# Performance work log

Hardware: AMD Instinct MI355X
Metric: run time of the kernel (lower is better)

## Reference

```python
import jax, jax.numpy as jnp
import numpy as np

B, L, D, N, K = 4, 4096, 1024, 64, 3
EPS = 1e-6

def setup_inputs() -> dict:
    key = jax.random.key(0)
    ks = jax.random.split(key, 24)
    f32 = jnp.float32
    inp = {
        'T': jax.random.normal(ks[0], (B, L, D), f32),
        'norm_scale': jnp.ones((D,), f32),
        'in_w': jax.random.normal(ks[1], (2 * D, D), f32) * (1.0 / np.sqrt(D)),
        'in_b': jnp.zeros((2 * D,), f32),
        'dw_w': jax.random.normal(ks[2], (D, 1, K), f32) * (1.0 / np.sqrt(K)),
        'dw_b': jnp.zeros((D,), f32),
        'pw_w': jax.random.normal(ks[3], (D, D), f32) * (1.0 / np.sqrt(D)),
        'pw_b': jnp.zeros((D,), f32),
        'f_win': jax.random.normal(ks[4], (N, D), f32) * (1.0 / np.sqrt(D)),
        'f_wout': jax.random.normal(ks[5], (D, N), f32) * (1.0 / np.sqrt(N)),
        'f_logA': jax.random.normal(ks[6], (N,), f32) * 0.02,
        'f_B': jax.random.normal(ks[7], (N,), f32) * 0.02,
        'f_C': jax.random.normal(ks[8], (N,), f32) * 0.02,
        'f_logdt': jnp.array(0.0, f32),
        'b_win': jax.random.normal(ks[9], (N, D), f32) * (1.0 / np.sqrt(D)),
        'b_wout': jax.random.normal(ks[10], (D, N), f32) * (1.0 / np.sqrt(N)),
        'b_logA': jax.random.normal(ks[11], (N,), f32) * 0.02,
        'b_B': jax.random.normal(ks[12], (N,), f32) * 0.02,
        'b_C': jax.random.normal(ks[13], (N,), f32) * 0.02,
        'b_logdt': jnp.array(0.0, f32),
        'out_w': jax.random.normal(ks[14], (D, D), f32) * (1.0 / np.sqrt(D)),
        'out_b': jnp.zeros((D,), f32),
    }
    return inp

def _ssm(x, win, wout, logA, Bp, Cp, logdt):
    # ZOH discretization of diagonal SSM
    dt = jnp.exp(logdt)
    A = -jnp.exp(logA)
    Abar = jnp.exp(A * dt)
    denom = jnp.where(jnp.abs(A) < EPS, jnp.ones_like(A), A)
    frac = jnp.where(jnp.abs(A) < EPS, dt, (Abar - 1.0) / denom)
    Bbar = frac * Bp
    u = jnp.einsum('bld,nd->bln', x, win)  # (B,L,N)
    h0 = jnp.zeros((x.shape[0], win.shape[0]), x.dtype)
    def step(h, ut):
        h = h * Abar + ut * Bbar
        return h, h * Cp
    _, ys = jax.lax.scan(step, h0, jnp.swapaxes(u, 0, 1))  # (L,B,N)
    y = jnp.swapaxes(ys, 0, 1)
    return jnp.einsum('bln,dn->bld', y, wout)

def reference(T, norm_scale, in_w, in_b, dw_w, dw_b, pw_w, pw_b,
              f_win, f_wout, f_logA, f_B, f_C, f_logdt,
              b_win, b_wout, b_logA, b_B, b_C, b_logdt,
              out_w, out_b):
    # RMSNorm
    rms = jnp.sqrt(jnp.mean(T * T, axis=-1, keepdims=True) + EPS)
    Tn = T / rms * norm_scale
    # in_linear -> chunk
    xz = Tn @ in_w.T + in_b
    x, z = jnp.split(xz, 2, axis=-1)
    gate = jax.nn.sigmoid(z)
    # depthwise-separable conv1d (NCH layout)
    xc = jnp.swapaxes(x, 1, 2)  # (B,D,L)
    xc = jax.lax.conv_general_dilated(
        xc, dw_w, window_strides=(1,), padding=[(K // 2, K // 2)],
        dimension_numbers=('NCH', 'OIH', 'NCH'), feature_group_count=D)
    xc = xc + dw_b[None, :, None]
    xc = jnp.einsum('bdl,ed->bel', xc, pw_w) + pw_b[None, :, None]
    x_conv = jnp.swapaxes(xc, 1, 2)  # (B,L,D)
    # bidirectional SSM
    y_f = _ssm(x_conv, f_win, f_wout, f_logA, f_B, f_C, f_logdt)
    y_b = _ssm(jnp.flip(x_conv, axis=1), b_win, b_wout, b_logA, b_B, b_C, b_logdt)
    y_b = jnp.flip(y_b, axis=1)
    y = (y_f + y_b) * gate
    y = y @ out_w.T + out_b
    return T + y
```

## Files before the change

### kernel.cpp

```cpp
#include <hip/hip_runtime.h>
#include <cstdint>


#define L_SEQ 4096
#define D_DIM 1024
#define B_SZ 4
#define M_TOK (B_SZ * L_SEQ)
#define CHUNKS 64
#define CLEN (L_SEQ / CHUNKS)

typedef short bf16x8 __attribute__((ext_vector_type(8)));
typedef float floatx4 __attribute__((ext_vector_type(4)));

__device__ inline unsigned short f2bf(float f) {
  union { float f; unsigned int u; } v; v.f = f;
  unsigned int r = v.u + 0x7FFFu + ((v.u >> 16) & 1u);
  return (unsigned short)(r >> 16);
}
__device__ inline float bf2f(unsigned short h) {
  union { unsigned int u; float f; } v; v.u = ((unsigned int)h) << 16;
  return v.f;
}

__device__ inline void load_lds16(const unsigned short* g, unsigned short* l) {
  __builtin_amdgcn_global_load_lds(
      (const __attribute__((address_space(1))) unsigned int*)g,
      (__attribute__((address_space(3))) unsigned int*)l, 16, 0, 0);
}

__global__ __launch_bounds__(256) void rmsnorm_kernel(
    const float* __restrict__ T, const float* __restrict__ scale,
    unsigned short* __restrict__ Tn) {
  int tok = blockIdx.x;
  int t = threadIdx.x;
  const float4* row = (const float4*)(T + (size_t)tok * D_DIM);
  float4 v = row[t];
  float ss = v.x*v.x + v.y*v.y + v.z*v.z + v.w*v.w;
  #pragma unroll
  for (int off = 32; off > 0; off >>= 1) ss += __shfl_down(ss, off);
  __shared__ float part[4];
  if ((t & 63) == 0) part[t >> 6] = ss;
  __syncthreads();
  float total = part[0] + part[1] + part[2] + part[3];
  float rinv = rsqrtf(total * (1.0f / D_DIM) + 1e-6f);
  const float4* sc4 = (const float4*)scale;
  float4 s = sc4[t];
  ushort4 o;
  o.x = f2bf(v.x * rinv * s.x); o.y = f2bf(v.y * rinv * s.y);
  o.z = f2bf(v.z * rinv * s.z); o.w = f2bf(v.w * rinv * s.w);
  ((ushort4*)(Tn + (size_t)tok * D_DIM))[t] = o;
}

__global__ __launch_bounds__(256) void f2bf_vec_kernel(
    const float* __restrict__ in, unsigned short* __restrict__ out, int n4) {
  int i = blockIdx.x * 256 + threadIdx.x;
  if (i < n4) {
    float4 v = ((const float4*)in)[i];
    ushort4 o; o.x = f2bf(v.x); o.y = f2bf(v.y); o.z = f2bf(v.z); o.w = f2bf(v.w);
    ((ushort4*)out)[i] = o;
  }
}

__global__ void prepack_kernel(
    const float* __restrict__ f_win, const float* __restrict__ b_win,
    const float* __restrict__ f_wout, const float* __restrict__ b_wout,
    unsigned short* __restrict__ Wu, unsigned short* __restrict__ Wy) {
  int i = blockIdx.x * blockDim.x + threadIdx.x;
  if (i < 128 * D_DIM) {
    int n = i >> 10, k = i & (D_DIM - 1);
    Wu[i] = f2bf((n < 64) ? f_win[n * D_DIM + k] : b_win[(n - 64) * D_DIM + k]);
    int d = i >> 7, kk = i & 127;
    Wy[i] = f2bf((kk < 64) ? f_wout[d * 64 + kk] : b_wout[d * 64 + (kk - 64)]);
  }
}

template<int MODE, typename OUT_T>
__global__ __launch_bounds__(256) void gemm_mfma_kernel(
    const unsigned short* __restrict__ A, const unsigned short* __restrict__ Bw,
    const float* __restrict__ bias, OUT_T* __restrict__ out,
    int M, int N, int Kt,
    const float* __restrict__ aux0, float* __restrict__ aux1) {
  __shared__ unsigned short As[128 * 32];
  __shared__ unsigned short Bs[128 * 32];
  int tid = threadIdx.x;
  int wave = tid >> 6, lane = tid & 63;
  int quad = lane >> 4, lrow = lane & 15;
  int bm = blockIdx.x * 128, bn = blockIdx.y * 128;
  int wm = (wave & 1) * 64, wn = (wave >> 1) * 64;

  int r0 = tid >> 2;
  int c8 = (tid & 3) * 8;
  const unsigned short* Ag0 = A  + (size_t)(bm + r0) * Kt + c8;
  const unsigned short* Ag1 = A  + (size_t)(bm + 64 + r0) * Kt + c8;
  const unsigned short* Bg0 = Bw + (size_t)(bn + r0) * Kt + c8;
  const unsigned short* Bg1 = Bw + (size_t)(bn + 64 + r0) * Kt + c8;
  unsigned short* Al0 = As + (size_t)(wave * 64) * 8;
  unsigned short* Al1 = As + (size_t)(256 + wave * 64) * 8;
  unsigned short* Bl0 = Bs + (size_t)(wave * 64) * 8;
  unsigned short* Bl1 = Bs + (size_t)(256 + wave * 64) * 8;

  floatx4 acc[4][4] = {};
  for (int k0 = 0; k0 < Kt; k0 += 32) {
    load_lds16(Ag0 + k0, Al0);
    load_lds16(Ag1 + k0, Al1);
    load_lds16(Bg0 + k0, Bl0);
    load_lds16(Bg1 + k0, Bl1);
    __syncthreads();
    bf16x8 af[4], bfr[4];
    #pragma unroll
    for (int mi = 0; mi < 4; ++mi)
      af[mi] = *(const bf16x8*)(As + (wm + mi * 16 + lrow) * 32 + quad * 8);
    #pragma unroll
    for (int ni = 0; ni < 4; ++ni)
      bfr[ni] = *(const bf16x8*)(Bs + (wn + ni * 16 + lrow) * 32 + quad * 8);
    #pragma unroll
    for (int mi = 0; mi < 4; ++mi)
      #pragma unroll
      for (int ni = 0; ni < 4; ++ni)
        acc[mi][ni] = __builtin_amdgcn_mfma_f32_16x16x32_bf16(
            af[mi], bfr[ni], acc[mi][ni], 0, 0, 0);
    __syncthreads();
  }

  #pragma unroll
  for (int mi = 0; mi < 4; ++mi) {
    #pragma unroll
    for (int ni = 0; ni < 4; ++ni) {
      #pragma unroll
      for (int r = 0; r < 4; ++r) {
        int m = bm + wm + mi * 16 + quad * 4 + r;
        int n = bn + wn + ni * 16 + lrow;
        float v = acc[mi][ni][r];
        if (MODE == 0) {
          if (bias) v += bias[n];
          if (sizeof(OUT_T) == 2) out[(size_t)m * N + n] = (OUT_T)f2bf(v);
          else                    out[(size_t)m * N + n] = (OUT_T)v;
        } else if (MODE == 1) {
          if (bias) v += bias[n];
          if (n < D_DIM) ((unsigned short*)out)[(size_t)m * D_DIM + n] = f2bf(v);
          else aux1[(size_t)m * D_DIM + (n - D_DIM)] = 1.0f / (1.0f + expf(-v));
        } else if (MODE == 2) {
          v *= aux0[(size_t)m * N + n];
          ((unsigned short*)out)[(size_t)m * N + n] = f2bf(v);
        } else {
          if (bias) v += bias[n];
          v += aux0[(size_t)m * N + n];
          ((float*)out)[(size_t)m * N + n] = v;
        }
      }
    }
  }
}

__global__ __launch_bounds__(256) void dwconv_kernel(
    const unsigned short* __restrict__ x, const float* __restrict__ w,
    const float* __restrict__ b, unsigned short* __restrict__ out) {
  size_t i8 = (size_t)blockIdx.x * 256 + threadIdx.x;
  int d8 = (int)(i8 & (D_DIM / 8 - 1));
  size_t tok = i8 >> 7;
  int l = (int)(tok & (L_SEQ - 1));
  int d0 = d8 * 8;
  size_t base = tok * D_DIM + d0;
  bf16x8 cur = *(const bf16x8*)(x + base);
  float acc[8];
  #pragma unroll
  for (int j = 0; j < 8; ++j) {
    int d = d0 + j;
    acc[j] = b[d] + w[d * 3 + 1] * bf2f((unsigned short)cur[j]);
  }
  if (l > 0) {
    bf16x8 prv = *(const bf16x8*)(x + base - D_DIM);
    #pragma unroll
    for (int j = 0; j < 8; ++j) acc[j] += w[(d0 + j) * 3 + 0] * bf2f((unsigned short)prv[j]);
  }
  if (l < L_SEQ - 1) {
    bf16x8 nxt = *(const bf16x8*)(x + base + D_DIM);
    #pragma unroll
    for (int j = 0; j < 8; ++j) acc[j] += w[(d0 + j) * 3 + 2] * bf2f((unsigned short)nxt[j]);
  }
  bf16x8 o;
  #pragma unroll
  for (int j = 0; j < 8; ++j) o[j] = (short)f2bf(acc[j]);
  *(bf16x8*)(out + base) = o;
}

__device__ inline void ssm_params(
    int col,
    const float* f_logA, const float* f_B, const float* f_C, const float* f_logdt,
    const float* b_logA, const float* b_B, const float* b_C, const float* b_logdt,
    float& Abar, float& Bbar, float& Cc, float& Aa, float& dt) {
  int dir = col >> 6, n = col & 63;
  const float* logA  = dir ? b_logA  : f_logA;
  const float* Bp    = dir ? b_B     : f_B;
  const float* Cp    = dir ? b_C     : f_C;
  const float* logdt = dir ? b_logdt : f_logdt;
  dt = expf(logdt[0]);
  Aa = -expf(logA[n]);
  Abar = expf(Aa * dt);
  float frac = (fabsf(Aa) < 1e-6f) ? dt : (Abar - 1.0f) / Aa;
  Bbar = frac * Bp[n];
  Cc = Cp[n];
}

__global__ __launch_bounds__(128) void scan_s1_kernel(
    const float* __restrict__ u, float* __restrict__ states,
    const float* __restrict__ f_logA, const float* __restrict__ f_B,
    const float* __restrict__ f_C, const float* __restrict__ f_logdt,
    const float* __restrict__ b_logA, const float* __restrict__ b_B,
    const float* __restrict__ b_C, const float* __restrict__ b_logdt) {
  int col = threadIdx.x;
  int chunk = blockIdx.x, b = blockIdx.y;
  float Abar, Bbar, Cc, Aa, dt;
  ssm_params(col, f_logA, f_B, f_C, f_logdt, b_logA, b_B, b_C, b_logdt,
             Abar, Bbar, Cc, Aa, dt);
  size_t base = ((size_t)b * L_SEQ + (size_t)chunk * CLEN) * 128 + col;
  float h = 0.0f;
  if (col < 64) {
    for (int i0 = 0; i0 < CLEN; i0 += 8) {
      float uv[8];
      #pragma unroll
      for (int j = 0; j < 8; ++j) uv[j] = u[base + (size_t)(i0 + j) * 128];
      #pragma unroll
      for (int j = 0; j < 8; ++j) h = h * Abar + uv[j] * Bbar;
    }
  } else {
    for (int i0 = CLEN - 1; i0 >= 0; i0 -= 8) {
      float uv[8];
      #pragma unroll
      for (int j = 0; j < 8; ++j) uv[j] = u[base + (size_t)(i0 - j) * 128];
      #pragma unroll
      for (int j = 0; j < 8; ++j) h = h * Abar + uv[j] * Bbar;
    }
  }
  states[((size_t)b * CHUNKS + chunk) * 128 + col] = h;
}

__global__ __launch_bounds__(512) void scan_s2_kernel(
    const float* __restrict__ states, float* __restrict__ carries,
    const float* __restrict__ f_logA, const float* __restrict__ f_B,
    const float* __restrict__ f_C, const float* __restrict__ f_logdt,
    const float* __restrict__ b_logA, const float* __restrict__ b_B,
    const float* __restrict__ b_C, const float* __restrict__ b_logdt) {
  int tid = threadIdx.x;
  int b = tid >> 7, col = tid & 127;
  float Abar, Bbar, Cc, Aa, dt;
  ssm_params(col, f_logA, f_B, f_C, f_logdt, b_logA, b_B, b_C, b_logdt,
             Abar, Bbar, Cc, Aa, dt);
  float Ac = expf(Aa * dt * (float)CLEN);
  size_t sb = (size_t)b * CHUNKS * 128 + col;
  float cur = 0.0f;
  if (col < 64) {
    for (int c = 0; c < CHUNKS; ++c) {
      carries[sb + (size_t)c * 128] = cur;
      cur = cur * Ac + states[sb + (size_t)c * 128];
    }
  } else {
    for (int c = CHUNKS - 1; c >= 0; --c) {
      carries[sb + (size_t)c * 128] = cur;
      cur = cur * Ac + states[sb + (size_t)c * 128];
    }
  }
}

__global__ __launch_bounds__(128) void scan_s3_kernel(
    const float* __restrict__ u, const float* __restrict__ carries,
    unsigned short* __restrict__ y,
    const float* __restrict__ f_logA, const float* __restrict__ f_B,
    const float* __restrict__ f_C, const float* __restrict__ f_logdt,
    const float* __restrict__ b_logA, const float* __restrict__ b_B,
    const float* __restrict__ b_C, const float* __restrict__ b_logdt) {
  int col = threadIdx.x;
  int chunk = blockIdx.x, b = blockIdx.y;
  float Abar, Bbar, Cc, Aa, dt;
  ssm_params(col, f_logA, f_B, f_C, f_logdt, b_logA, b_B, b_C, b_logdt,
             Abar, Bbar, Cc, Aa, dt);
  size_t base = ((size_t)b * L_SEQ + (size_t)chunk * CLEN) * 128 + col;
  float h = carries[((size_t)b * CHUNKS + chunk) * 128 + col];
  if (col < 64) {
    for (int i0 = 0; i0 < CLEN; i0 += 8) {
      float uv[8];
      #pragma unroll
      for (int j = 0; j < 8; ++j) uv[j] = u[base + (size_t)(i0 + j) * 128];
      #pragma unroll
      for (int j = 0; j < 8; ++j) {
        h = h * Abar + uv[j] * Bbar;
        y[base + (size_t)(i0 + j) * 128] = f2bf(h * Cc);
      }
    }
  } else {
    for (int i0 = CLEN - 1; i0 >= 0; i0 -= 8) {
      float uv[8];
      #pragma unroll
      for (int j = 0; j < 8; ++j) uv[j] = u[base + (size_t)(i0 - j) * 128];
      #pragma unroll
      for (int j = 0; j < 8; ++j) {
        h = h * Abar + uv[j] * Bbar;
        y[base + (size_t)(i0 - j) * 128] = f2bf(h * Cc);
      }
    }
  }
}

extern "C" void kernel_launch(void* const* d_in, const int* in_sizes, int n_in,
                              void* d_out, int out_size, void* d_ws, size_t ws_size,
                              hipStream_t stream) {
  const float* T         = (const float*)d_in[0];
  const float* norm_scale= (const float*)d_in[1];
  const float* in_w      = (const float*)d_in[2];
  const float* in_b      = (const float*)d_in[3];
  const float* dw_w      = (const float*)d_in[4];
  const float* dw_b      = (const float*)d_in[5];
  const float* pw_w      = (const float*)d_in[6];
  const float* pw_b      = (const float*)d_in[7];
  const float* f_win     = (const float*)d_in[8];
  const float* f_wout    = (const float*)d_in[9];
  const float* f_logA    = (const float*)d_in[10];
  const float* f_B       = (const float*)d_in[11];
  const float* f_C       = (const float*)d_in[12];
  const float* f_logdt   = (const float*)d_in[13];
  const float* b_win     = (const float*)d_in[14];
  const float* b_wout    = (const float*)d_in[15];
  const float* b_logA    = (const float*)d_in[16];
  const float* b_B       = (const float*)d_in[17];
  const float* b_C       = (const float*)d_in[18];
  const float* b_logdt   = (const float*)d_in[19];
  const float* out_w     = (const float*)d_in[20];
  const float* out_b     = (const float*)d_in[21];
  float* out = (float*)d_out;

  char* ws = (char*)d_ws;
  const size_t MD = (size_t)M_TOK * D_DIM;
  float*          gate  = (float*)ws;                       ws += MD * 4;
  unsigned short* bufA  = (unsigned short*)ws;              ws += MD * 2;
  unsigned short* bufB  = (unsigned short*)ws;              ws += MD * 2;
  float*          u     = (float*)ws;                       ws += (size_t)M_TOK * 128 * 4;
  unsigned short* ybuf  = (unsigned short*)ws;              ws += (size_t)M_TOK * 128 * 2;
  unsigned short* w_in  = (unsigned short*)ws;              ws += (size_t)2 * D_DIM * D_DIM * 2;
  unsigned short* w_pw  = (unsigned short*)ws;              ws += (size_t)D_DIM * D_DIM * 2;
  unsigned short* w_out = (unsigned short*)ws;              ws += (size_t)D_DIM * D_DIM * 2;
  unsigned short* Wu    = (unsigned short*)ws;              ws += (size_t)128 * D_DIM * 2;
  unsigned short* Wy    = (unsigned short*)ws;              ws += (size_t)128 * D_DIM * 2;
  float*          states= (float*)ws;                       ws += (size_t)B_SZ * CHUNKS * 128 * 4;
  float*          carries=(float*)ws;

  f2bf_vec_kernel<<<(2 * D_DIM * D_DIM / 4 + 255) / 256, 256, 0, stream>>>(in_w, w_in, 2 * D_DIM * D_DIM / 4);
  f2bf_vec_kernel<<<(D_DIM * D_DIM / 4 + 255) / 256, 256, 0, stream>>>(pw_w, w_pw, D_DIM * D_DIM / 4);
  f2bf_vec_kernel<<<(D_DIM * D_DIM / 4 + 255) / 256, 256, 0, stream>>>(out_w, w_out, D_DIM * D_DIM / 4);
  prepack_kernel<<<(128 * D_DIM) / 256, 256, 0, stream>>>(f_win, b_win, f_wout, b_wout, Wu, Wy);
  rmsnorm_kernel<<<M_TOK, 256, 0, stream>>>(T, norm_scale, bufA);
  {
    dim3 g(M_TOK / 128, (2 * D_DIM) / 128);
    gemm_mfma_kernel<1, unsigned short><<<g, 256, 0, stream>>>(
        bufA, w_in, in_b, bufB, M_TOK, 2 * D_DIM, D_DIM, nullptr, gate);
  }
  dwconv_kernel<<<(MD / 8) / 256, 256, 0, stream>>>(bufB, dw_w, dw_b, bufA);
  {
    dim3 g(M_TOK / 128, D_DIM / 128);
    gemm_mfma_kernel<0, unsigned short><<<g, 256, 0, stream>>>(
        bufA, w_pw, pw_b, bufB, M_TOK, D_DIM, D_DIM, nullptr, nullptr);
  }
  {
    dim3 g(M_TOK / 128, 1);
    gemm_mfma_kernel<0, float><<<g, 256, 0, stream>>>(
        bufB, Wu, nullptr, u, M_TOK, 128, D_DIM, nullptr, nullptr);
  }
  {
    dim3 g1(CHUNKS, B_SZ);
    scan_s1_kernel<<<g1, 128, 0, stream>>>(u, states, f_logA, f_B, f_C, f_logdt,
                                           b_logA, b_B, b_C, b_logdt);
    scan_s2_kernel<<<1, 512, 0, stream>>>(states, carries, f_logA, f_B, f_C, f_logdt,
                                          b_logA, b_B, b_C, b_logdt);
    scan_s3_kernel<<<g1, 128, 0, stream>>>(u, carries, ybuf, f_logA, f_B, f_C, f_logdt,
                                           b_logA, b_B, b_C, b_logdt);
  }
  {
    dim3 g(M_TOK / 128, D_DIM / 128);
    gemm_mfma_kernel<2, unsigned short><<<g, 256, 0, stream>>>(
        ybuf, Wy, nullptr, bufA, M_TOK, D_DIM, 128, gate, nullptr);
  }
  {
    dim3 g(M_TOK / 128, D_DIM / 128);
    gemm_mfma_kernel<3, float><<<g, 256, 0, stream>>>(
        bufA, w_out, out_b, out, M_TOK, D_DIM, D_DIM, T, nullptr);
  }
}
```

Before: 643.0 us.

## Double GEMM K-step, swap grid axes, and store gate in bf16

The MFMA GEMM now loads a 64-wide K slab per iteration (two 32-wide LDS sub-tiles), which halves the number of barrier pairs per tile. The grid is transposed so consecutive blocks share the same A row-block and walk across N, which should improve L2 reuse of activations. The sigmoid gate is stored as bf16 instead of fp32, halving its write and read traffic at a small precision cost. LDS use per block doubles, which may limit occupancy.

New measurement: 636.9 us. No clear change (-1.0%).

```diff
diff --git a/kernel.cpp b/kernel.cpp
--- a/kernel.cpp
+++ b/kernel.cpp
@@ -79,13 +79,13 @@
     const unsigned short* __restrict__ A, const unsigned short* __restrict__ Bw,
     const float* __restrict__ bias, OUT_T* __restrict__ out,
     int M, int N, int Kt,
-    const float* __restrict__ aux0, float* __restrict__ aux1) {
-  __shared__ unsigned short As[128 * 32];
-  __shared__ unsigned short Bs[128 * 32];
+    const void* __restrict__ aux0, unsigned short* __restrict__ aux1) {
+  __shared__ unsigned short As[2 * 128 * 32];
+  __shared__ unsigned short Bs[2 * 128 * 32];
   int tid = threadIdx.x;
   int wave = tid >> 6, lane = tid & 63;
   int quad = lane >> 4, lrow = lane & 15;
-  int bm = blockIdx.x * 128, bn = blockIdx.y * 128;
+  int bm = blockIdx.y * 128, bn = blockIdx.x * 128;
   int wm = (wave & 1) * 64, wn = (wave >> 1) * 64;
 
   int r0 = tid >> 2;
@@ -94,31 +94,40 @@
   const unsigned short* Ag1 = A  + (size_t)(bm + 64 + r0) * Kt + c8;
   const unsigned short* Bg0 = Bw + (size_t)(bn + r0) * Kt + c8;
   const unsigned short* Bg1 = Bw + (size_t)(bn + 64 + r0) * Kt + c8;
-  unsigned short* Al0 = As + (size_t)(wave * 64) * 8;
-  unsigned short* Al1 = As + (size_t)(256 + wave * 64) * 8;
-  unsigned short* Bl0 = Bs + (size_t)(wave * 64) * 8;
-  unsigned short* Bl1 = Bs + (size_t)(256 + wave * 64) * 8;
+  unsigned short* Al0 = As + (size_t)wave * 512;
+  unsigned short* Al1 = As + 2048 + (size_t)wave * 512;
+  unsigned short* Bl0 = Bs + (size_t)wave * 512;
+  unsigned short* Bl1 = Bs + 2048 + (size_t)wave * 512;
 
   floatx4 acc[4][4] = {};
-  for (int k0 = 0; k0 < Kt; k0 += 32) {
+  for (int k0 = 0; k0 < Kt; k0 += 64) {
     load_lds16(Ag0 + k0, Al0);
     load_lds16(Ag1 + k0, Al1);
     load_lds16(Bg0 + k0, Bl0);
     load_lds16(Bg1 + k0, Bl1);
+    load_lds16(Ag0 + k0 + 32, Al0 + 4096);
+    load_lds16(Ag1 + k0 + 32, Al1 + 4096);
+    load_lds16(Bg0 + k0 + 32, Bl0 + 4096);
+    load_lds16(Bg1 + k0 + 32, Bl1 + 4096);
     __syncthreads();
-    bf16x8 af[4], bfr[4];
     #pragma unroll
-    for (int mi = 0; mi < 4; ++mi)
-      af[mi] = *(const bf16x8*)(As + (wm + mi * 16 + lrow) * 32 + quad * 8);
-    #pragma unroll
-    for (int ni = 0; ni < 4; ++ni)
-      bfr[ni] = *(const bf16x8*)(Bs + (wn + ni * 16 + lrow) * 32 + quad * 8);
-    #pragma unroll
-    for (int mi = 0; mi < 4; ++mi)
+    for (int ks = 0; ks < 2; ++ks) {
+      const unsigned short* Ab = As + ks * 4096;
+      const unsigned short* Bb = Bs + ks * 4096;
+      bf16x8 af[4], bfr[4];
+      #pragma unroll
+      for (int mi = 0; mi < 4; ++mi)
+        af[mi] = *(const bf16x8*)(Ab + (wm + mi * 16 + lrow) * 32 + quad * 8);
       #pragma unroll
       for (int ni = 0; ni < 4; ++ni)
-        acc[mi][ni] = __builtin_amdgcn_mfma_f32_16x16x32_bf16(
-            af[mi], bfr[ni], acc[mi][ni], 0, 0, 0);
+        bfr[ni] = *(const bf16x8*)(Bb + (wn + ni * 16 + lrow) * 32 + quad * 8);
+      #pragma unroll
+      for (int mi = 0; mi < 4; ++mi)
+        #pragma unroll
+        for (int ni = 0; ni < 4; ++ni)
+          acc[mi][ni] = __builtin_amdgcn_mfma_f32_16x16x32_bf16(
+              af[mi], bfr[ni], acc[mi][ni], 0, 0, 0);
+    }
     __syncthreads();
   }
 
@@ -138,13 +147,13 @@
         } else if (MODE == 1) {
           if (bias) v += bias[n];
           if (n < D_DIM) ((unsigned short*)out)[(size_t)m * D_DIM + n] = f2bf(v);
-          else aux1[(size_t)m * D_DIM + (n - D_DIM)] = 1.0f / (1.0f + expf(-v));
+          else aux1[(size_t)m * D_DIM + (n - D_DIM)] = f2bf(1.0f / (1.0f + expf(-v)));
         } else if (MODE == 2) {
-          v *= aux0[(size_t)m * N + n];
+          v *= bf2f(((const unsigned short*)aux0)[(size_t)m * N + n]);
           ((unsigned short*)out)[(size_t)m * N + n] = f2bf(v);
         } else {
           if (bias) v += bias[n];
-          v += aux0[(size_t)m * N + n];
+          v += ((const float*)aux0)[(size_t)m * N + n];
           ((float*)out)[(size_t)m * N + n] = v;
         }
       }
@@ -330,7 +339,7 @@
 
   char* ws = (char*)d_ws;
   const size_t MD = (size_t)M_TOK * D_DIM;
-  float*          gate  = (float*)ws;                       ws += MD * 4;
+  unsigned short* gate  = (unsigned short*)ws;              ws += MD * 2;
   unsigned short* bufA  = (unsigned short*)ws;              ws += MD * 2;
   unsigned short* bufB  = (unsigned short*)ws;              ws += MD * 2;
   float*          u     = (float*)ws;                       ws += (size_t)M_TOK * 128 * 4;
@@ -349,18 +358,18 @@
   prepack_kernel<<<(128 * D_DIM) / 256, 256, 0, stream>>>(f_win, b_win, f_wout, b_wout, Wu, Wy);
   rmsnorm_kernel<<<M_TOK, 256, 0, stream>>>(T, norm_scale, bufA);
   {
-    dim3 g(M_TOK / 128, (2 * D_DIM) / 128);
+    dim3 g((2 * D_DIM) / 128, M_TOK / 128);
     gemm_mfma_kernel<1, unsigned short><<<g, 256, 0, stream>>>(
         bufA, w_in, in_b, bufB, M_TOK, 2 * D_DIM, D_DIM, nullptr, gate);
   }
   dwconv_kernel<<<(MD / 8) / 256, 256, 0, stream>>>(bufB, dw_w, dw_b, bufA);
   {
-    dim3 g(M_TOK / 128, D_DIM / 128);
+    dim3 g(D_DIM / 128, M_TOK / 128);
     gemm_mfma_kernel<0, unsigned short><<<g, 256, 0, stream>>>(
         bufA, w_pw, pw_b, bufB, M_TOK, D_DIM, D_DIM, nullptr, nullptr);
   }
   {
-    dim3 g(M_TOK / 128, 1);
+    dim3 g(1, M_TOK / 128);
     gemm_mfma_kernel<0, float><<<g, 256, 0, stream>>>(
         bufB, Wu, nullptr, u, M_TOK, 128, D_DIM, nullptr, nullptr);
   }
@@ -374,12 +383,12 @@
                                            b_logA, b_B, b_C, b_logdt);
   }
   {
-    dim3 g(M_TOK / 128, D_DIM / 128);
+    dim3 g(D_DIM / 128, M_TOK / 128);
     gemm_mfma_kernel<2, unsigned short><<<g, 256, 0, stream>>>(
         ybuf, Wy, nullptr, bufA, M_TOK, D_DIM, 128, gate, nullptr);
   }
   {
-    dim3 g(M_TOK / 128, D_DIM / 128);
+    dim3 g(D_DIM / 128, M_TOK / 128);
     gemm_mfma_kernel<3, float><<<g, 256, 0, stream>>>(
         bufA, w_out, out_b, out, M_TOK, D_DIM, D_DIM, T, nullptr);
   }
```

## Fold pointwise conv weights into SSM input projection; store gate as bf16

Applied to the files above, without the earlier changes.

The pointwise 1024x1024 conv GEMM is removed by precomputing Wcomb = win·pw_w and a bias ucomb = win·pw_b. The dwconv output then feeds the 128-wide u projection directly. This drops a full M×D×D GEMM and its intermediate buffer, at the cost of a small serial weight-combination kernel. The gate is also stored as bf16 instead of fp32 to halve its traffic, which adds some rounding error.

Result: slower. 731.4 us (+13.8%).

```diff
diff --git a/kernel.cpp b/kernel.cpp
--- a/kernel.cpp
+++ b/kernel.cpp
@@ -61,17 +61,44 @@
   }
 }
 
-__global__ void prepack_kernel(
-    const float* __restrict__ f_win, const float* __restrict__ b_win,
+__global__ void prepack_wy_kernel(
     const float* __restrict__ f_wout, const float* __restrict__ b_wout,
-    unsigned short* __restrict__ Wu, unsigned short* __restrict__ Wy) {
+    unsigned short* __restrict__ Wy) {
   int i = blockIdx.x * blockDim.x + threadIdx.x;
   if (i < 128 * D_DIM) {
-    int n = i >> 10, k = i & (D_DIM - 1);
-    Wu[i] = f2bf((n < 64) ? f_win[n * D_DIM + k] : b_win[(n - 64) * D_DIM + k]);
     int d = i >> 7, kk = i & 127;
     Wy[i] = f2bf((kk < 64) ? f_wout[d * 64 + kk] : b_wout[d * 64 + (kk - 64)]);
   }
+}
+
+__global__ __launch_bounds__(256) void wcomb_kernel(
+    const float* __restrict__ f_win, const float* __restrict__ b_win,
+    const float* __restrict__ pw_w, unsigned short* __restrict__ Wcomb) {
+  int n0 = blockIdx.x * 8;
+  int d = blockIdx.y * 256 + threadIdx.x;
+  const float* w = (n0 < 64) ? f_win : b_win;
+  int nb = n0 & 63;
+  float acc[8] = {0,0,0,0,0,0,0,0};
+  for (int e = 0; e < D_DIM; ++e) {
+    float p = pw_w[(size_t)e * D_DIM + d];
+    #pragma unroll
+    for (int j = 0; j < 8; ++j)
+      acc[j] += w[(nb + j) * D_DIM + e] * p;
+  }
+  #pragma unroll
+  for (int j = 0; j < 8; ++j)
+    Wcomb[(size_t)(n0 + j) * D_DIM + d] = f2bf(acc[j]);
+}
+
+__global__ __launch_bounds__(128) void ucomb_kernel(
+    const float* __restrict__ f_win, const float* __restrict__ b_win,
+    const float* __restrict__ pw_b, float* __restrict__ ucomb) {
+  int n = threadIdx.x;
+  const float* w = (n < 64) ? f_win : b_win;
+  int nb = n & 63;
+  float acc = 0.0f;
+  for (int e = 0; e < D_DIM; ++e) acc += w[nb * D_DIM + e] * pw_b[e];
+  ucomb[n] = acc;
 }
 
 template<int MODE, typename OUT_T>
@@ -79,7 +106,7 @@
     const unsigned short* __restrict__ A, const unsigned short* __restrict__ Bw,
     const float* __restrict__ bias, OUT_T* __restrict__ out,
     int M, int N, int Kt,
-    const float* __restrict__ aux0, float* __restrict__ aux1) {
+    const void* __restrict__ aux0, unsigned short* __restrict__ aux1) {
   __shared__ unsigned short As[128 * 32];
   __shared__ unsigned short Bs[128 * 32];
   int tid = threadIdx.x;
@@ -138,13 +165,13 @@
         } else if (MODE == 1) {
           if (bias) v += bias[n];
           if (n < D_DIM) ((unsigned short*)out)[(size_t)m * D_DIM + n] = f2bf(v);
-          else aux1[(size_t)m * D_DIM + (n - D_DIM)] = 1.0f / (1.0f + expf(-v));
+          else aux1[(size_t)m * D_DIM + (n - D_DIM)] = f2bf(1.0f / (1.0f + expf(-v)));
         } else if (MODE == 2) {
-          v *= aux0[(size_t)m * N + n];
+          v *= bf2f(((const unsigned short*)aux0)[(size_t)m * N + n]);
           ((unsigned short*)out)[(size_t)m * N + n] = f2bf(v);
         } else {
           if (bias) v += bias[n];
-          v += aux0[(size_t)m * N + n];
+          v += ((const float*)aux0)[(size_t)m * N + n];
           ((float*)out)[(size_t)m * N + n] = v;
         }
       }
@@ -330,23 +357,27 @@
 
   char* ws = (char*)d_ws;
   const size_t MD = (size_t)M_TOK * D_DIM;
-  float*          gate  = (float*)ws;                       ws += MD * 4;
+  unsigned short* gate  = (unsigned short*)ws;              ws += MD * 2;
   unsigned short* bufA  = (unsigned short*)ws;              ws += MD * 2;
   unsigned short* bufB  = (unsigned short*)ws;              ws += MD * 2;
   float*          u     = (float*)ws;                       ws += (size_t)M_TOK * 128 * 4;
   unsigned short* ybuf  = (unsigned short*)ws;              ws += (size_t)M_TOK * 128 * 2;
   unsigned short* w_in  = (unsigned short*)ws;              ws += (size_t)2 * D_DIM * D_DIM * 2;
-  unsigned short* w_pw  = (unsigned short*)ws;              ws += (size_t)D_DIM * D_DIM * 2;
   unsigned short* w_out = (unsigned short*)ws;              ws += (size_t)D_DIM * D_DIM * 2;
-  unsigned short* Wu    = (unsigned short*)ws;              ws += (size_t)128 * D_DIM * 2;
+  unsigned short* Wcomb = (unsigned short*)ws;              ws += (size_t)128 * D_DIM * 2;
   unsigned short* Wy    = (unsigned short*)ws;              ws += (size_t)128 * D_DIM * 2;
+  float*          ucomb = (float*)ws;                       ws += 128 * 4;
   float*          states= (float*)ws;                       ws += (size_t)B_SZ * CHUNKS * 128 * 4;
   float*          carries=(float*)ws;
 
   f2bf_vec_kernel<<<(2 * D_DIM * D_DIM / 4 + 255) / 256, 256, 0, stream>>>(in_w, w_in, 2 * D_DIM * D_DIM / 4);
-  f2bf_vec_kernel<<<(D_DIM * D_DIM / 4 + 255) / 256, 256, 0, stream>>>(pw_w, w_pw, D_DIM * D_DIM / 4);
   f2bf_vec_kernel<<<(D_DIM * D_DIM / 4 + 255) / 256, 256, 0, stream>>>(out_w, w_out, D_DIM * D_DIM / 4);
-  prepack_kernel<<<(128 * D_DIM) / 256, 256, 0, stream>>>(f_win, b_win, f_wout, b_wout, Wu, Wy);
+  prepack_wy_kernel<<<(128 * D_DIM) / 256, 256, 0, stream>>>(f_wout, b_wout, Wy);
+  {
+    dim3 g(16, 4);
+    wcomb_kernel<<<g, 256, 0, stream>>>(f_win, b_win, pw_w, Wcomb);
+  }
+  ucomb_kernel<<<1, 128, 0, stream>>>(f_win, b_win, pw_b, ucomb);
   rmsnorm_kernel<<<M_TOK, 256, 0, stream>>>(T, norm_scale, bufA);
   {
     dim3 g(M_TOK / 128, (2 * D_DIM) / 128);
@@ -355,14 +386,9 @@
   }
   dwconv_kernel<<<(MD / 8) / 256, 256, 0, stream>>>(bufB, dw_w, dw_b, bufA);
   {
-    dim3 g(M_TOK / 128, D_DIM / 128);
-    gemm_mfma_kernel<0, unsigned short><<<g, 256, 0, stream>>>(
-        bufA, w_pw, pw_b, bufB, M_TOK, D_DIM, D_DIM, nullptr, nullptr);
-  }
-  {
     dim3 g(M_TOK / 128, 1);
     gemm_mfma_kernel<0, float><<<g, 256, 0, stream>>>(
-        bufB, Wu, nullptr, u, M_TOK, 128, D_DIM, nullptr, nullptr);
+        bufA, Wcomb, ucomb, u, M_TOK, 128, D_DIM, nullptr, nullptr);
   }
   {
     dim3 g1(CHUNKS, B_SZ);
```
